# Kernel tuning notes

Hardware: AMD Instinct MI355X
Metric: run time of the kernel (lower is better)

Reference implementation:

```python
import jax, jax.numpy as jnp
import numpy as np

W_BITS = 4  # active precision (max of supported_bits)
EPS = 0.005  # clamp margin from the original module


def _dequant_kbit(qweight, lut, w_bits):
    """Bit-plane LUT dequant.
    qweight: [w_bits, O, I//32] int32, plane b holds bit b (MSB-first code) of each
    weight's k-bit index, 32 consecutive input positions per int32 word (LSB-first
    within a word). lut: [O, 2**w_bits]. Returns dense weight [O, I].
    """
    O = qweight.shape[1]
    shifts = jnp.arange(32, dtype=jnp.int32)                     # bit position within word
    bits = (qweight[:, :, :, None] >> shifts) & 1                # [w_bits, O, I//32, 32]
    plane_w = (1 << (w_bits - 1 - jnp.arange(w_bits, dtype=jnp.int32)))
    idx = (bits * plane_w[:, None, None, None]).sum(axis=0)      # [O, I//32, 32]
    idx = idx.reshape(O, -1)                                     # [O, I]
    return jnp.take_along_axis(lut, idx, axis=1)                 # [O, I]


def _csr_dense(rows, cols, vals, O, I):
    """Scatter CSR (indptr=rows) into a dense [O, I] matrix."""
    nnz = cols.shape[0]
    k = jnp.arange(nnz, dtype=rows.dtype)
    row_ids = jnp.searchsorted(rows, k, side='right') - 1        # CSR row of each nnz
    return jnp.zeros((O, I), dtype=vals.dtype).at[row_ids, cols].add(vals)


def setup_inputs() -> dict:
    key = jax.random.key(0)
    ks = jax.random.split(key, 7)
    B, S, I, O = 4, 2048, 4096, 4096
    NNZ = 65536
    x = jax.random.normal(ks[0], (B, S, I), dtype=jnp.float32)
    qweight = jax.random.randint(ks[1], (W_BITS, O, I // 32), 0, 2147483647, dtype=jnp.int32)
    lut = jax.random.normal(ks[2], (O, 2 ** W_BITS), dtype=jnp.float32) * 0.05
    rows = jnp.sort(jax.random.randint(ks[3], (O + 1,), 0, NNZ, dtype=jnp.int32))
    rows = rows.at[0].set(0).at[-1].set(NNZ)                     # valid CSR indptr
    cols = jax.random.randint(ks[4], (NNZ,), 0, I, dtype=jnp.int32)
    vals = jax.random.normal(ks[5], (NNZ,), dtype=jnp.float32) * 0.01
    bias = jax.random.normal(ks[6], (O,), dtype=jnp.float32) * 0.01
    return {"x": x, "qweight": qweight, "lut": lut, "rows": rows,
            "cols": cols, "vals": vals, "bias": bias}


def reference(x, qweight, lut, rows, cols, vals, bias):
    O = qweight.shape[1]
    I = x.shape[-1]
    weight = _dequant_kbit(qweight, lut, W_BITS)                 # [O, I]
    y = jnp.einsum('bsi,oi->bso', x, weight)                     # dense quantized GEMM
    w_sp = _csr_dense(rows, cols, vals, O, I)                    # sparse outlier weights
    y = y + jnp.einsum('bsi,oi->bso', x, w_sp)
    y = y + bias
    fmax = jnp.finfo(x.dtype).max * (1.0 - EPS)
    return jnp.clip(y, -fmax, fmax)
```

## Files before the change

kernel.cpp:

```cpp
#include <hip/hip_runtime.h>
#include <stdint.h>

#define Mdim 8192
#define Ndim 4096
#define Kdim 4096

#define BM 256
#define BN 256
#define BK 32
#define NT (Kdim / BK)

typedef float f32x4 __attribute__((ext_vector_type(4)));
typedef __bf16 bf16x8 __attribute__((ext_vector_type(8)));
typedef unsigned short ushort_t;

#define FMAXC 3.3858093490333422e+38f

__device__ __forceinline__ ushort_t f2bf(float f) {
    unsigned u = __float_as_uint(f);
    u += 0x7fffu + ((u >> 16) & 1u);
    return (ushort_t)(u >> 16);
}

__device__ __forceinline__ void gload_lds16(const void* g, void* l) {
    __builtin_amdgcn_global_load_lds(
        (const __attribute__((address_space(1))) uint32_t*)g,
        (__attribute__((address_space(3))) uint32_t*)(uint32_t)(uintptr_t)l,
        16, 0, 0);
}

__global__ __launch_bounds__(128) void dequant_kernel(
        const int* __restrict__ qw, const float* __restrict__ lut,
        const int* __restrict__ rows, const int* __restrict__ cols,
        const float* __restrict__ vals, ushort_t* __restrict__ w16) {
    __shared__ float wrow[128 * 33];
    __shared__ float slut[16];
    const int o = blockIdx.x;
    const int t = threadIdx.x;

    if (t < 16) slut[t] = lut[o * 16 + t];
    __syncthreads();

    const int q0 = qw[0 * Ndim * 128 + o * 128 + t];
    const int q1 = qw[1 * Ndim * 128 + o * 128 + t];
    const int q2 = qw[2 * Ndim * 128 + o * 128 + t];
    const int q3 = qw[3 * Ndim * 128 + o * 128 + t];
    float* dst = &wrow[t * 33];
#pragma unroll
    for (int j = 0; j < 32; ++j) {
        int idx = (((q0 >> j) & 1) << 3) | (((q1 >> j) & 1) << 2) |
                  (((q2 >> j) & 1) << 1) | ((q3 >> j) & 1);
        dst[j] = slut[idx];
    }
    __syncthreads();

    const int beg = rows[o], end = rows[o + 1];
    for (int k = beg + t; k < end; k += 128) {
        int c = cols[k];
        atomicAdd(&wrow[c + (c >> 5)], vals[k]);
    }
    __syncthreads();

    __align__(16) ushort_t tmp[32];
#pragma unroll
    for (int j = 0; j < 32; ++j) tmp[j] = f2bf(dst[j]);
    uint4* dstg = (uint4*)(w16 + (size_t)o * Kdim + t * 32);
    const uint4* srcg = (const uint4*)tmp;
#pragma unroll
    for (int j = 0; j < 4; ++j) dstg[j] = srcg[j];
}

__global__ __launch_bounds__(256) void convx_kernel(
        const float* __restrict__ x, ushort_t* __restrict__ y) {
    size_t i = ((size_t)blockIdx.x * 256 + threadIdx.x) * 8;
    float4 a = *(const float4*)(x + i);
    float4 b = *(const float4*)(x + i + 4);
    __align__(16) ushort_t r[8] = {f2bf(a.x), f2bf(a.y), f2bf(a.z), f2bf(a.w),
                                   f2bf(b.x), f2bf(b.y), f2bf(b.z), f2bf(b.w)};
    *(uint4*)(y + i) = *(const uint4*)r;
}

__global__ __launch_bounds__(512, 2) void gemm_kernel(
        const ushort_t* __restrict__ A, const ushort_t* __restrict__ Bw,
        const float* __restrict__ bias, float* __restrict__ C) {
    __shared__ __align__(16) char lds[131072];

    const int wgid = blockIdx.x;
    const int swz = (wgid & 7) * 64 + (wgid >> 3);
    const int bn = swz & 15, bm = swz >> 4;
    const int m0 = bm * BM, n0 = bn * BN;

    const int tid = threadIdx.x;
    const int lane = tid & 63, wid = tid >> 6;
    const int wr = wid >> 2, wc = wid & 3;
    const int fr = lane & 15, kg = lane >> 4;

    const int sline = tid >> 3;
    const int slot = (tid & 7) ^ (sline & 7);
    const int srow0 = (sline << 1) + (slot >> 2);
    const int skel = (slot & 3) * 8;
    const ushort_t* gA = A + (size_t)(m0 + srow0) * Kdim + skel;
    const ushort_t* gB = Bw + (size_t)(n0 + srow0) * Kdim + skel;

    const int offL = (fr >> 1) * 128 + (((((fr & 1) << 2) | kg) ^ (fr >> 1)) << 4);

    f32x4 acc[8][4];
#pragma unroll
    for (int i = 0; i < 8; ++i)
#pragma unroll
        for (int j = 0; j < 4; ++j) acc[i][j] = (f32x4){0.f, 0.f, 0.f, 0.f};

    const ushort_t* pA = gA;
    const ushort_t* pB = gB;

    auto stageA = [&](int bufd) {
        char* d = lds + bufd * 16384 + tid * 16;
        gload_lds16(pA, d);
        gload_lds16(pA + (size_t)128 * Kdim, d + 8192);
    };
    auto stageB = [&](int bufd) {
        char* d = lds + 65536 + bufd * 16384 + tid * 16;
        gload_lds16(pB, d);
        gload_lds16(pB + (size_t)128 * Kdim, d + 8192);
    };

    stageA(0); stageB(0); pA += BK; pB += BK;
    stageA(1); stageB(1); pA += BK; pB += BK;
    asm volatile("s_waitcnt vmcnt(4)" ::: "memory");
    asm volatile("s_barrier" ::: "memory");

#pragma unroll 1
    for (int t = 0; t < NT; ++t) {
        const int bufi = t & 3;
        const int buf2 = (t + 2) & 3;
        const char* Ab = lds + bufi * 16384;
        const char* Bb = lds + 65536 + bufi * 16384;

        if (t + 2 < NT) {
            stageA(buf2);
            stageB(buf2);
        }
        pA += BK; pB += BK;

        bf16x8 Af[8], Bf[4];
#pragma unroll
        for (int n = 0; n < 4; ++n) {
            Af[n] = *(const bf16x8*)(Ab + wr * 8192 + n * 1024 + offL);
            Bf[n] = *(const bf16x8*)(Bb + wc * 4096 + n * 1024 + offL);
        }
#pragma unroll
        for (int m = 4; m < 8; ++m)
            Af[m] = *(const bf16x8*)(Ab + wr * 8192 + m * 1024 + offL);

        __builtin_amdgcn_s_setprio(1);
#pragma unroll
        for (int m = 0; m < 4; ++m)
#pragma unroll
            for (int n = 0; n < 4; ++n)
                acc[m][n] = __builtin_amdgcn_mfma_f32_16x16x32_bf16(
                    Af[m], Bf[n], acc[m][n], 0, 0, 0);
#pragma unroll
        for (int m = 4; m < 8; ++m)
#pragma unroll
            for (int n = 0; n < 4; ++n)
                acc[m][n] = __builtin_amdgcn_mfma_f32_16x16x32_bf16(
                    Af[m], Bf[n], acc[m][n], 0, 0, 0);
        __builtin_amdgcn_s_setprio(0);

        if (t < NT - 2) {
            asm volatile("s_waitcnt vmcnt(4)" ::: "memory");
        } else if (t == NT - 2) {
            asm volatile("s_waitcnt vmcnt(0)" ::: "memory");
        }
        asm volatile("s_barrier" ::: "memory");
    }

    const int rg = lane >> 4;
#pragma unroll
    for (int nf = 0; nf < 4; ++nf) {
        const int col = n0 + wc * 64 + nf * 16 + fr;
        const float bv = bias[col];
#pragma unroll
        for (int mf = 0; mf < 8; ++mf) {
            const int row = m0 + wr * 128 + mf * 16 + rg * 4;
            float* outp = C + (size_t)row * Ndim + col;
#pragma unroll
            for (int j = 0; j < 4; ++j) {
                float v = acc[mf][nf][j] + bv;
                v = fminf(fmaxf(v, -FMAXC), FMAXC);
                outp[(size_t)j * Ndim] = v;
            }
        }
    }
}

extern "C" void kernel_launch(void* const* d_in, const int* in_sizes, int n_in,
                              void* d_out, int out_size, void* d_ws, size_t ws_size,
                              hipStream_t stream) {
    const float* x    = (const float*)d_in[0];
    const int*   qw   = (const int*)d_in[1];
    const float* lut  = (const float*)d_in[2];
    const int*   rows = (const int*)d_in[3];
    const int*   cols = (const int*)d_in[4];
    const float* vals = (const float*)d_in[5];
    const float* bias = (const float*)d_in[6];
    float* out = (float*)d_out;

    ushort_t* x16 = (ushort_t*)d_ws;
    ushort_t* w16 = x16 + (size_t)Mdim * Kdim;

    hipLaunchKernelGGL(dequant_kernel, dim3(Ndim), dim3(128), 0, stream,
                       qw, lut, rows, cols, vals, w16);
    hipLaunchKernelGGL(convx_kernel, dim3((Mdim * Kdim) / (256 * 8)), dim3(256), 0, stream,
                       x, x16);
    hipLaunchKernelGGL(gemm_kernel, dim3((Mdim / BM) * (Ndim / BN)), dim3(512), 0, stream,
                       x16, w16, bias, out);
}
```

Before: 292.4 us.

## Software-pipeline LDS fragment reads with MFMA halves in GEMM main loop

Restructures the GEMM main loop into a ping-pong schedule. LDS fragment reads for the next tile (A-lo and B) and for the current tile's upper A half are issued while MFMAs on already loaded fragments run. Global-to-LDS staging of A and B is split across the two half-phases, with finer vmcnt/lgkmcnt waits and extra barriers. The loop is unrolled by two with an explicit epilogue for the last two tiles. The aim is to hide LDS read latency behind MFMA work, at the cost of more registers, more barriers and delicate manual waitcnt accounting.

```diff
diff --git a/kernel.cpp b/kernel.cpp
--- a/kernel.cpp
+++ b/kernel.cpp
@@ -117,62 +117,106 @@
         char* d = lds + bufd * 16384 + tid * 16;
         gload_lds16(pA, d);
         gload_lds16(pA + (size_t)128 * Kdim, d + 8192);
+        pA += BK;
     };
     auto stageB = [&](int bufd) {
         char* d = lds + 65536 + bufd * 16384 + tid * 16;
         gload_lds16(pB, d);
         gload_lds16(pB + (size_t)128 * Kdim, d + 8192);
-    };
-
-    stageA(0); stageB(0); pA += BK; pB += BK;
-    stageA(1); stageB(1); pA += BK; pB += BK;
-    asm volatile("s_waitcnt vmcnt(4)" ::: "memory");
-    asm volatile("s_barrier" ::: "memory");
+        pB += BK;
+    };
+    auto readAlo = [&](bf16x8 (&FA)[4], int buf) {
+#pragma unroll
+        for (int m = 0; m < 4; ++m)
+            FA[m] = *(const bf16x8*)(lds + buf * 16384 + wr * 8192 + m * 1024 + offL);
+    };
+    auto readAhi = [&](bf16x8 (&FA)[4], int buf) {
+#pragma unroll
+        for (int m = 0; m < 4; ++m)
+            FA[m] = *(const bf16x8*)(lds + buf * 16384 + wr * 8192 + (m + 4) * 1024 + offL);
+    };
+    auto readB = [&](bf16x8 (&FB)[4], int buf) {
+#pragma unroll
+        for (int n = 0; n < 4; ++n)
+            FB[n] = *(const bf16x8*)(lds + 65536 + buf * 16384 + wc * 4096 + n * 1024 + offL);
+    };
+    auto mfmaHalf = [&](int mb, bf16x8 (&FA)[4], bf16x8 (&FB)[4]) {
+        __builtin_amdgcn_s_setprio(1);
+#pragma unroll
+        for (int m = 0; m < 4; ++m)
+#pragma unroll
+            for (int n = 0; n < 4; ++n)
+                acc[mb + m][n] = __builtin_amdgcn_mfma_f32_16x16x32_bf16(
+                    FA[m], FB[n], acc[mb + m][n], 0, 0, 0);
+        __builtin_amdgcn_s_setprio(0);
+    };
+
+    bf16x8 Ac[4], An[4], BA[4], BB[4];
+
+    auto tileMain = [&](int t, bf16x8 (&Bc)[4], bf16x8 (&Bn)[4]) {
+        const int bufR = t & 3, bufR1 = (t + 1) & 3, bufS = (t + 2) & 3;
+        readAhi(An, bufR);
+        stageA(bufS);
+        asm volatile("s_waitcnt vmcnt(2)");
+        __builtin_amdgcn_sched_barrier(0);
+        __builtin_amdgcn_s_barrier();
+        asm volatile("s_waitcnt lgkmcnt(4)");
+        __builtin_amdgcn_sched_barrier(0);
+        mfmaHalf(0, Ac, Bc);
+        __builtin_amdgcn_s_barrier();
+        readAlo(Ac, bufR1);
+        readB(Bn, bufR1);
+        stageB(bufS);
+        __builtin_amdgcn_sched_barrier(0);
+        __builtin_amdgcn_s_barrier();
+        asm volatile("s_waitcnt lgkmcnt(8)");
+        __builtin_amdgcn_sched_barrier(0);
+        mfmaHalf(4, An, Bc);
+        __builtin_amdgcn_s_barrier();
+    };
+
+    stageA(0); stageB(0);
+    stageA(1); stageB(1);
+    asm volatile("s_waitcnt vmcnt(4)");
+    __builtin_amdgcn_sched_barrier(0);
+    __builtin_amdgcn_s_barrier();
+    readAlo(Ac, 0);
+    readB(BA, 0);
 
 #pragma unroll 1
-    for (int t = 0; t < NT; ++t) {
-        const int bufi = t & 3;
-        const int buf2 = (t + 2) & 3;
-        const char* Ab = lds + bufi * 16384;
-        const char* Bb = lds + 65536 + bufi * 16384;
-
-        if (t + 2 < NT) {
-            stageA(buf2);
-            stageB(buf2);
-        }
-        pA += BK; pB += BK;
-
-        bf16x8 Af[8], Bf[4];
-#pragma unroll
-        for (int n = 0; n < 4; ++n) {
-            Af[n] = *(const bf16x8*)(Ab + wr * 8192 + n * 1024 + offL);
-            Bf[n] = *(const bf16x8*)(Bb + wc * 4096 + n * 1024 + offL);
-        }
-#pragma unroll
-        for (int m = 4; m < 8; ++m)
-            Af[m] = *(const bf16x8*)(Ab + wr * 8192 + m * 1024 + offL);
-
-        __builtin_amdgcn_s_setprio(1);
-#pragma unroll
-        for (int m = 0; m < 4; ++m)
-#pragma unroll
-            for (int n = 0; n < 4; ++n)
-                acc[m][n] = __builtin_amdgcn_mfma_f32_16x16x32_bf16(
-                    Af[m], Bf[n], acc[m][n], 0, 0, 0);
-#pragma unroll
-        for (int m = 4; m < 8; ++m)
-#pragma unroll
-            for (int n = 0; n < 4; ++n)
-                acc[m][n] = __builtin_amdgcn_mfma_f32_16x16x32_bf16(
-                    Af[m], Bf[n], acc[m][n], 0, 0, 0);
-        __builtin_amdgcn_s_setprio(0);
-
-        if (t < NT - 2) {
-            asm volatile("s_waitcnt vmcnt(4)" ::: "memory");
-        } else if (t == NT - 2) {
-            asm volatile("s_waitcnt vmcnt(0)" ::: "memory");
-        }
-        asm volatile("s_barrier" ::: "memory");
+    for (int t = 0; t < NT - 2; t += 2) {
+        tileMain(t, BA, BB);
+        tileMain(t + 1, BB, BA);
+    }
+
+    {
+        const int bufR = (NT - 2) & 3, bufR1 = (NT - 1) & 3;
+        readAhi(An, bufR);
+        asm volatile("s_waitcnt vmcnt(0)");
+        __builtin_amdgcn_sched_barrier(0);
+        __builtin_amdgcn_s_barrier();
+        asm volatile("s_waitcnt lgkmcnt(4)");
+        __builtin_amdgcn_sched_barrier(0);
+        mfmaHalf(0, Ac, BA);
+        __builtin_amdgcn_s_barrier();
+        readAlo(Ac, bufR1);
+        readB(BB, bufR1);
+        __builtin_amdgcn_sched_barrier(0);
+        __builtin_amdgcn_s_barrier();
+        asm volatile("s_waitcnt lgkmcnt(8)");
+        __builtin_amdgcn_sched_barrier(0);
+        mfmaHalf(4, An, BA);
+        __builtin_amdgcn_s_barrier();
+    }
+    {
+        const int bufR = (NT - 1) & 3;
+        readAhi(An, bufR);
+        asm volatile("s_waitcnt lgkmcnt(4)");
+        __builtin_amdgcn_sched_barrier(0);
+        mfmaHalf(0, Ac, BB);
+        asm volatile("s_waitcnt lgkmcnt(0)");
+        __builtin_amdgcn_sched_barrier(0);
+        mfmaHalf(4, An, BB);
     }
 
     const int rg = lane >> 4;
```

After: 302.9 us. 1.04x slower.
